# Performance work log

Hardware: AMD Instinct MI355X
Metric: run time of the kernel (lower is better)

## Reference

```python
import jax, jax.numpy as jnp
import numpy as np

D = 2048
NUM_EXPERTS = 64
TOP_K = 4
G = 8            # sqrt(num_experts)
K_PER_G = 8      # num_experts // G
G_ACTIVE = 2     # sqrt(top_k)
K_PER_G_ACTIVE = 2  # top_k // g_active


def setup_inputs() -> dict:
    key = jax.random.key(0)
    kx, k1, k2 = jax.random.split(key, 3)
    x = jax.random.normal(kx, (4, 8192, D), dtype=jnp.float32)
    # nn.Linear(d, G, bias=False) weight shape [G, d]; Linear(d, K_per_g) -> [K_per_g, d]
    W1 = jax.random.normal(k1, (G, D), dtype=jnp.float32) * 0.02
    W2 = jax.random.normal(k2, (K_PER_G, D), dtype=jnp.float32) * 0.02
    return {"x": x, "W1": W1, "W2": W2}


def reference(x, W1, W2):
    # Level-1: group scores [B, S, G], pick top g_active groups
    g_scores = jnp.einsum("bsd,gd->bsg", x, W1)
    top_g_scores, top_g_idx = jax.lax.top_k(g_scores, G_ACTIVE)
    # Level-2: within-group expert scores [B, S, K_per_g], pick top k_per_g_active
    e_scores = jnp.einsum("bsd,kd->bsk", x, W2)
    top_e_scores, top_e_idx = jax.lax.top_k(e_scores, K_PER_G_ACTIVE)
    # Combine indices: global = g * K_per_g + e, via broadcasting -> [B,S,g_active,k_per_g_active]
    global_idx = top_g_idx[..., :, None] * K_PER_G + top_e_idx[..., None, :]
    topk_idx = global_idx.reshape(*global_idx.shape[:-2], TOP_K)
    # Combine scores additively and re-softmax over the top_k slots
    combined = top_g_scores[..., :, None] + top_e_scores[..., None, :]
    combined = combined.reshape(*combined.shape[:-2], TOP_K)
    weights = jax.nn.softmax(combined, axis=-1)
    return topk_idx, weights
```

## Files before the change

kernel.cpp:

```cpp
#include <hip/hip_runtime.h>
#include <math.h>


#define D       2048
#define NTOK    32768
#define IDX_REG 131072

template <int T>
__device__ __forceinline__ void load_sc(const float (&acc)[16][4], float (&sc)[16]) {
#pragma unroll
    for (int k = 0; k < 16; ++k) sc[k] = acc[k][T];
}

__global__ __launch_bounds__(256, 2) void router_kernel(
    const float* __restrict__ x,
    const float* __restrict__ W1,
    const float* __restrict__ W2,
    float* __restrict__ out)
{
    const int lane = threadIdx.x & 63;
    const int wave = (blockIdx.x << 2) | (threadIdx.x >> 6);
    const int g    = lane >> 4;
    const int j    = lane & 15;
    const int tok_base = wave * 16 + g * 4;

    float acc[16][4];
#pragma unroll
    for (int k = 0; k < 16; ++k)
#pragma unroll
        for (int t = 0; t < 4; ++t) acc[k][t] = 0.f;

    const float* xbase = x + (size_t)tok_base * D + (j << 2);

    for (int s = 0; s < 32; ++s) {
        const int d = s * 64 + (j << 2);

        float4 xv[4];
#pragma unroll
        for (int t = 0; t < 4; ++t)
            xv[t] = *(const float4*)(xbase + t * D + s * 64);

        float4 wv[8];
#pragma unroll
        for (int k = 0; k < 8; ++k)
            wv[k] = *(const float4*)(W1 + k * D + d);
#pragma unroll
        for (int k = 0; k < 8; ++k)
#pragma unroll
            for (int t = 0; t < 4; ++t) {
                acc[k][t] = fmaf(wv[k].x, xv[t].x, acc[k][t]);
                acc[k][t] = fmaf(wv[k].y, xv[t].y, acc[k][t]);
                acc[k][t] = fmaf(wv[k].z, xv[t].z, acc[k][t]);
                acc[k][t] = fmaf(wv[k].w, xv[t].w, acc[k][t]);
            }

#pragma unroll
        for (int k = 0; k < 8; ++k)
            wv[k] = *(const float4*)(W2 + k * D + d);
#pragma unroll
        for (int k = 0; k < 8; ++k)
#pragma unroll
            for (int t = 0; t < 4; ++t) {
                acc[8 + k][t] = fmaf(wv[k].x, xv[t].x, acc[8 + k][t]);
                acc[8 + k][t] = fmaf(wv[k].y, xv[t].y, acc[8 + k][t]);
                acc[8 + k][t] = fmaf(wv[k].z, xv[t].z, acc[8 + k][t]);
                acc[8 + k][t] = fmaf(wv[k].w, xv[t].w, acc[8 + k][t]);
            }
    }

#pragma unroll
    for (int m = 1; m <= 8; m <<= 1)
#pragma unroll
        for (int k = 0; k < 16; ++k)
#pragma unroll
            for (int t = 0; t < 4; ++t)
                acc[k][t] += __shfl_xor(acc[k][t], m, 64);

    if (j < 4) {
        float sc[16];
        if      (j == 0) load_sc<0>(acc, sc);
        else if (j == 1) load_sc<1>(acc, sc);
        else if (j == 2) load_sc<2>(acc, sc);
        else             load_sc<3>(acc, sc);

        const int token = tok_base + j;

        float bg0 = sc[0]; int gi0 = 0; float bg1 = -INFINITY; int gi1 = 0;
#pragma unroll
        for (int k = 1; k < 8; ++k) {
            float v = sc[k];
            if (v > bg0) { bg1 = bg0; gi1 = gi0; bg0 = v; gi0 = k; }
            else if (v > bg1) { bg1 = v; gi1 = k; }
        }
        float be0 = sc[8]; int ei0 = 0; float be1 = -INFINITY; int ei1 = 0;
#pragma unroll
        for (int k = 1; k < 8; ++k) {
            float v = sc[8 + k];
            if (v > be0) { be1 = be0; ei1 = ei0; be0 = v; ei0 = k; }
            else if (v > be1) { be1 = v; ei1 = k; }
        }

        float c0 = bg0 + be0, c1 = bg0 + be1, c2 = bg1 + be0, c3 = bg1 + be1;
        float e0 = 1.f;
        float e1 = __expf(c1 - c0);
        float e2 = __expf(c2 - c0);
        float e3 = __expf(c3 - c0);
        float inv = 1.f / (e0 + e1 + e2 + e3);

        float4 idxv = make_float4((float)(gi0 * 8 + ei0), (float)(gi0 * 8 + ei1),
                                  (float)(gi1 * 8 + ei0), (float)(gi1 * 8 + ei1));
        float4 wout = make_float4(e0 * inv, e1 * inv, e2 * inv, e3 * inv);

        *(float4*)(out + (size_t)token * 4)           = idxv;
        *(float4*)(out + IDX_REG + (size_t)token * 4) = wout;
    }
}

extern "C" void kernel_launch(void* const* d_in, const int* in_sizes, int n_in,
                              void* d_out, int out_size, void* d_ws, size_t ws_size,
                              hipStream_t stream) {
    const float* x  = (const float*)d_in[0];
    const float* W1 = (const float*)d_in[1];
    const float* W2 = (const float*)d_in[2];
    float* out = (float*)d_out;
    dim3 grid(512), block(256);
    hipLaunchKernelGGL(router_kernel, grid, block, 0, stream, x, W1, W2, out);
}
```

Before: 386.6 us.

## Stage router weights in LDS, use nontemporal x loads, larger blocks

Each 512-thread block copies W1 and W2 (128 KB) into shared memory once, and the inner loop reads the 16 weight rows from LDS instead of global/L1. Loads of x use nontemporal hints so the streaming input does not pollute cache, and the loop is unrolled by 2. The grid drops to 256 blocks of 512 threads. The 128 KB of LDS per block limits occupancy and adds a preload and barrier per block, and the larger weight register array raises register pressure.

Result: faster. 342.6 us (-11.4%).

```diff
diff --git a/kernel.cpp b/kernel.cpp
--- a/kernel.cpp
+++ b/kernel.cpp
@@ -6,23 +6,41 @@
 #define NTOK    32768
 #define IDX_REG 131072
 
+typedef float f4 __attribute__((ext_vector_type(4)));
+
 template <int T>
 __device__ __forceinline__ void load_sc(const float (&acc)[16][4], float (&sc)[16]) {
 #pragma unroll
     for (int k = 0; k < 16; ++k) sc[k] = acc[k][T];
 }
 
-__global__ __launch_bounds__(256, 2) void router_kernel(
+__global__ __launch_bounds__(512, 2) void router_kernel(
     const float* __restrict__ x,
     const float* __restrict__ W1,
     const float* __restrict__ W2,
     float* __restrict__ out)
 {
-    const int lane = threadIdx.x & 63;
-    const int wave = (blockIdx.x << 2) | (threadIdx.x >> 6);
+    __shared__ float w_lds[32768];
+
+    const int tid  = threadIdx.x;
+    const int lane = tid & 63;
     const int g    = lane >> 4;
     const int j    = lane & 15;
+    const int wave = (blockIdx.x << 3) | (tid >> 6);
     const int tok_base = wave * 16 + g * 4;
+
+    {
+        f4* lds4 = (f4*)w_lds;
+        const f4* w1v = (const f4*)W1;
+        const f4* w2v = (const f4*)W2;
+#pragma unroll
+        for (int i = 0; i < 8; ++i) {
+            int idx = tid + i * 512;
+            lds4[idx]        = w1v[idx];
+            lds4[4096 + idx] = w2v[idx];
+        }
+    }
+    __syncthreads();
 
     float acc[16][4];
 #pragma unroll
@@ -32,39 +50,28 @@
 
     const float* xbase = x + (size_t)tok_base * D + (j << 2);
 
+#pragma unroll 2
     for (int s = 0; s < 32; ++s) {
         const int d = s * 64 + (j << 2);
 
-        float4 xv[4];
+        f4 xv[4];
 #pragma unroll
         for (int t = 0; t < 4; ++t)
-            xv[t] = *(const float4*)(xbase + t * D + s * 64);
+            xv[t] = __builtin_nontemporal_load((const f4*)(xbase + t * D + s * 64));
 
-        float4 wv[8];
+        f4 wv[16];
 #pragma unroll
-        for (int k = 0; k < 8; ++k)
-            wv[k] = *(const float4*)(W1 + k * D + d);
+        for (int k = 0; k < 16; ++k)
+            wv[k] = *(const f4*)(w_lds + k * D + d);
+
 #pragma unroll
-        for (int k = 0; k < 8; ++k)
+        for (int k = 0; k < 16; ++k)
 #pragma unroll
             for (int t = 0; t < 4; ++t) {
                 acc[k][t] = fmaf(wv[k].x, xv[t].x, acc[k][t]);
                 acc[k][t] = fmaf(wv[k].y, xv[t].y, acc[k][t]);
                 acc[k][t] = fmaf(wv[k].z, xv[t].z, acc[k][t]);
                 acc[k][t] = fmaf(wv[k].w, xv[t].w, acc[k][t]);
-            }
-
-#pragma unroll
-        for (int k = 0; k < 8; ++k)
-            wv[k] = *(const float4*)(W2 + k * D + d);
-#pragma unroll
-        for (int k = 0; k < 8; ++k)
-#pragma unroll
-            for (int t = 0; t < 4; ++t) {
-                acc[8 + k][t] = fmaf(wv[k].x, xv[t].x, acc[8 + k][t]);
-                acc[8 + k][t] = fmaf(wv[k].y, xv[t].y, acc[8 + k][t]);
-                acc[8 + k][t] = fmaf(wv[k].z, xv[t].z, acc[8 + k][t]);
-                acc[8 + k][t] = fmaf(wv[k].w, xv[t].w, acc[8 + k][t]);
             }
     }
 
@@ -123,6 +130,6 @@
     const float* W1 = (const float*)d_in[1];
     const float* W2 = (const float*)d_in[2];
     float* out = (float*)d_out;
-    dim3 grid(512), block(256);
+    dim3 grid(256), block(512);
     hipLaunchKernelGGL(router_kernel, grid, block, 0, stream, x, W1, W2, out);
 }
```
